# Performance work log

Hardware: AMD Instinct MI355X
Metric: run time of the kernel (lower is better)

The kernel has to match this reference:

```python
import jax, jax.numpy as jnp
import numpy as np

N_NODES = 50000
N_EDGES = 800000
IN_DIM = 128
HIDDEN = 256
N_ETYPES = 13
N_STEPS = 6
NUM_GRAPHS = 64


def setup_inputs() -> dict:
    key = jax.random.key(0)
    ks = jax.random.split(key, 10)
    feat = jax.random.normal(ks[0], (N_NODES, IN_DIM), dtype=jnp.float32)
    W = jax.random.normal(ks[1], (N_ETYPES, HIDDEN, HIDDEN), dtype=jnp.float32) * 0.05
    W_ih = jax.random.normal(ks[2], (3 * HIDDEN, HIDDEN), dtype=jnp.float32) * 0.05
    W_hh = jax.random.normal(ks[3], (3 * HIDDEN, HIDDEN), dtype=jnp.float32) * 0.05
    b_ih = jnp.zeros((3 * HIDDEN,), dtype=jnp.float32)
    b_hh = jnp.zeros((3 * HIDDEN,), dtype=jnp.float32)
    Wc = jax.random.normal(ks[4], (1, HIDDEN), dtype=jnp.float32) * 0.05
    bc = jnp.zeros((1,), dtype=jnp.float32)
    src = jax.random.randint(ks[5], (N_EDGES,), 0, N_NODES, dtype=jnp.int32)
    dst = jax.random.randint(ks[6], (N_EDGES,), 0, N_NODES, dtype=jnp.int32)
    etype = jax.random.randint(ks[7], (N_EDGES,), 0, N_ETYPES, dtype=jnp.int32)
    graph_id = jnp.sort(jax.random.randint(ks[8], (N_NODES,), 0, NUM_GRAPHS, dtype=jnp.int32))
    return {"feat": feat, "W": W, "W_ih": W_ih, "W_hh": W_hh, "b_ih": b_ih,
            "b_hh": b_hh, "Wc": Wc, "bc": bc, "src": src, "dst": dst,
            "etype": etype, "graph_id": graph_id}


def reference(feat, W, W_ih, W_hh, b_ih, b_hh, Wc, bc, src, dst, etype, graph_id):
    N, H = feat.shape[0], W.shape[-1]
    # zero-pad input features to hidden size (DGL GatedGraphConv behaviour)
    h0 = jnp.concatenate([feat, jnp.zeros((N, H - feat.shape[1]), feat.dtype)], axis=1)

    def step(h, _):
        # per-etype linear transform of all nodes: [n_etypes, N, H]
        Th = jnp.einsum('nd,edf->enf', h, W)
        # gather transformed source feature per edge by its edge type: [E, H]
        msg = Th[etype, src]
        # scatter-sum aggregation into destination nodes: [N, H]
        a = jax.ops.segment_sum(msg, dst, num_segments=N)
        # torch.nn.GRUCell(a, h)
        gx = a @ W_ih.T + b_ih
        gh = h @ W_hh.T + b_hh
        xr, xz, xn = jnp.split(gx, 3, axis=-1)
        hr, hz, hn = jnp.split(gh, 3, axis=-1)
        r = jax.nn.sigmoid(xr + hr)
        z = jax.nn.sigmoid(xz + hz)
        n = jnp.tanh(xn + r * hn)
        return (1.0 - z) * n + z * h, None

    h, _ = jax.lax.scan(step, h0, None, length=N_STEPS)
    h = jax.nn.relu(h)
    # dgl.sum_nodes readout per graph: [num_graphs, H]
    hg = jax.ops.segment_sum(h, graph_id, num_segments=NUM_GRAPHS)
    out = jax.nn.sigmoid(hg @ Wc.T + bc)
    return out.squeeze(-1)
```

## Files before the change

kernel.cpp:

```cpp
#include <hip/hip_runtime.h>
#include <math.h>

#define N_NODES   50000
#define N_EDGES   800000
#define IN_DIM    128
#define HIDDEN    256
#define N_ETYPES  13
#define N_STEPS   6
#define NUM_GRAPHS 64
#define NKEYS     (N_ETYPES * N_NODES)
#define SCAN_T    512

typedef __attribute__((ext_vector_type(8))) short bf16x8;
typedef __attribute__((ext_vector_type(4))) float f32x4;
typedef __attribute__((ext_vector_type(4))) unsigned short u16x4;
typedef __attribute__((ext_vector_type(8))) _Float16 f16x8;
typedef __attribute__((ext_vector_type(4))) _Float16 f16x4;

__device__ __forceinline__ float bf2f(unsigned short u) {
    return __uint_as_float((unsigned)u << 16);
}
__device__ __forceinline__ void fsplit(float x, unsigned short& hi, unsigned short& lo) {
    unsigned u = __float_as_uint(x);
    hi = (unsigned short)(u >> 16);
    float l = x - __uint_as_float((u >> 16) << 16);
    lo = (unsigned short)(__float_as_uint(l) >> 16);
}

__global__ __launch_bounds__(256) void k_init_h(const float* __restrict__ feat,
                                                unsigned short* __restrict__ hHi,
                                                unsigned short* __restrict__ hLo,
                                                _Float16* __restrict__ hF16) {
    int i = blockIdx.x * 256 + threadIdx.x;
    if (i >= N_NODES * 64) return;
    int v = i >> 6;
    int q = i & 63;
    float4 val;
    if (q < 32) val = ((const float4*)(feat + (size_t)v * IN_DIM))[q];
    else        val = make_float4(0.f, 0.f, 0.f, 0.f);
    unsigned short h0, l0, h1, l1, h2, l2, h3, l3;
    fsplit(val.x, h0, l0);
    fsplit(val.y, h1, l1);
    fsplit(val.z, h2, l2);
    fsplit(val.w, h3, l3);
    u16x4 hi4, lo4;
    hi4[0] = h0; hi4[1] = h1; hi4[2] = h2; hi4[3] = h3;
    lo4[0] = l0; lo4[1] = l1; lo4[2] = l2; lo4[3] = l3;
    *(u16x4*)(hHi + (size_t)v * 256 + q * 4) = hi4;
    *(u16x4*)(hLo + (size_t)v * 256 + q * 4) = lo4;
    f16x4 f4;
    f4[0] = (_Float16)val.x; f4[1] = (_Float16)val.y;
    f4[2] = (_Float16)val.z; f4[3] = (_Float16)val.w;
    *(f16x4*)(hF16 + (size_t)v * 256 + q * 4) = f4;
}

__global__ __launch_bounds__(256) void k_splitW(const float* __restrict__ W,
                                                short* __restrict__ Whi,
                                                short* __restrict__ Wlo) {
    int i = blockIdx.x * 256 + threadIdx.x;
    if (i >= N_ETYPES * 65536) return;
    int t = i >> 16, rem = i & 65535, n = rem >> 8, k = rem & 255;
    float x = W[(size_t)t * 65536 + k * 256 + n];
    unsigned short hb, lb;
    fsplit(x, hb, lb);
    Whi[i] = (short)hb;
    Wlo[i] = (short)lb;
}

__global__ __launch_bounds__(256) void k_splitLin(const float* __restrict__ Wsrc,
                                                  short* __restrict__ hi,
                                                  short* __restrict__ lo, int n) {
    int i = blockIdx.x * 256 + threadIdx.x;
    if (i >= n) return;
    unsigned short hb, lb;
    fsplit(Wsrc[i], hb, lb);
    hi[i] = (short)hb;
    lo[i] = (short)lb;
}

__global__ __launch_bounds__(256) void k_hist(const int* __restrict__ dst,
                                              const int* __restrict__ et,
                                              int* __restrict__ counts) {
    int e = blockIdx.x * 256 + threadIdx.x;
    if (e >= N_EDGES) return;
    int key = et[e] * N_NODES + dst[e];
    atomicAdd(&counts[key], 1);
}

__global__ __launch_bounds__(SCAN_T) void k_scan1(const int* __restrict__ in,
                                                  int* __restrict__ lexcl,
                                                  int* __restrict__ bsums, int n) {
    __shared__ int s[SCAN_T];
    int i = blockIdx.x * SCAN_T + threadIdx.x;
    int v = (i < n) ? in[i] : 0;
    s[threadIdx.x] = v;
    __syncthreads();
    for (int off = 1; off < SCAN_T; off <<= 1) {
        int t = (threadIdx.x >= off) ? s[threadIdx.x - off] : 0;
        __syncthreads();
        s[threadIdx.x] += t;
        __syncthreads();
    }
    if (i < n) lexcl[i] = s[threadIdx.x] - v;
    if (threadIdx.x == SCAN_T - 1) bsums[blockIdx.x] = s[SCAN_T - 1];
}

__global__ __launch_bounds__(256) void k_scan2(int* __restrict__ bsums, int nb,
                                               int* __restrict__ ptr) {
    __shared__ int s[256];
    int tid = threadIdx.x;
    const int C = (nb + 255) / 256;
    int vals[8];
    int base = tid * C;
    int sum = 0;
    for (int i = 0; i < C; ++i) {
        int idx = base + i;
        int v = (idx < nb) ? bsums[idx] : 0;
        vals[i] = sum;
        sum += v;
    }
    s[tid] = sum;
    __syncthreads();
    int own = sum;
    for (int off = 1; off < 256; off <<= 1) {
        int t = (tid >= off) ? s[tid - off] : 0;
        __syncthreads();
        s[tid] += t;
        __syncthreads();
    }
    int exclBlk = s[tid] - own;
    for (int i = 0; i < C; ++i) {
        int idx = base + i;
        if (idx < nb) bsums[idx] = exclBlk + vals[i];
    }
    if (tid == 0) ptr[NKEYS] = N_EDGES;
}

__global__ __launch_bounds__(SCAN_T) void k_scan3(const int* __restrict__ lexcl,
                                                  const int* __restrict__ bsums,
                                                  int* __restrict__ ptr, int n) {
    int i = blockIdx.x * SCAN_T + threadIdx.x;
    if (i < n) ptr[i] = lexcl[i] + bsums[blockIdx.x];
}

__global__ __launch_bounds__(256) void k_place(const int* __restrict__ dst,
                                               const int* __restrict__ et,
                                               const int* __restrict__ src,
                                               int* __restrict__ cursor,
                                               unsigned* __restrict__ ebuf) {
    int e = blockIdx.x * 256 + threadIdx.x;
    if (e >= N_EDGES) return;
    int d = dst[e];
    int key = et[e] * N_NODES + d;
    int pos = atomicAdd(&cursor[key], 1);
    ebuf[pos] = ((unsigned)d << 16) | (unsigned)src[e];
}

__device__ __forceinline__ void split8(const float4& A, const float4& B,
                                       bf16x8& hi, bf16x8& lo) {
    float x[8] = {A.x, A.y, A.z, A.w, B.x, B.y, B.z, B.w};
    #pragma unroll
    for (int e = 0; e < 8; ++e) {
        unsigned short hb, lb;
        fsplit(x[e], hb, lb);
        hi[e] = (short)hb;
        lo[e] = (short)lb;
    }
}

__global__ __launch_bounds__(256, 4) void k_msg(const unsigned* __restrict__ ebuf,
                                                const int* __restrict__ ptr,
                                                const _Float16* __restrict__ hF16,
                                                const short* __restrict__ Whi,
                                                const short* __restrict__ Wlo,
                                                float* __restrict__ a) {
    __shared__ float4 Sh4[32 * 64];
    const int br   = blockIdx.x * 32;
    const int tid  = threadIdx.x;
    const int l    = tid & 63;
    const int w    = tid >> 6;
    const int ln15 = l & 15;
    const int lhi  = l >> 4;
    const int g    = tid >> 4;
    const int q    = tid & 15;
    float* shf = (float*)Sh4;

    f32x4 acc[2][4] = {};

    for (int t = 0; t < N_ETYPES; ++t) {
        float4 z4 = make_float4(0.f, 0.f, 0.f, 0.f);
        #pragma unroll
        for (int i = 0; i < 8; ++i) Sh4[tid + i * 256] = z4;
        __syncthreads();
        {
            int base = t * N_NODES + br;
            int endk = (br + 32 <= N_NODES) ? (base + 32) : (t * N_NODES + N_NODES);
            int beg  = ptr[base];
            int end  = ptr[endk];
            for (int i = beg + g; i < end; i += 16) {
                unsigned pk = ebuf[i];
                int s = (int)(pk & 0xFFFFu);
                int r = (int)(pk >> 16) - br;
                int sw = r & 7;
                #pragma unroll
                for (int j2 = 0; j2 < 2; ++j2) {
                    const _Float16* vp = hF16 + (size_t)s * 256 + j2 * 128 + q * 8;
                    f16x8 v8 = *reinterpret_cast<const f16x8*>(vp);
                    int c0 = (j2 * 32 + 2 * q) ^ sw;
                    int c1 = (j2 * 32 + 2 * q + 1) ^ sw;
                    float* p0 = shf + ((r * 64 + c0) << 2);
                    float* p1 = shf + ((r * 64 + c1) << 2);
                    atomicAdd(p0 + 0, (float)v8[0]);
                    atomicAdd(p0 + 1, (float)v8[1]);
                    atomicAdd(p0 + 2, (float)v8[2]);
                    atomicAdd(p0 + 3, (float)v8[3]);
                    atomicAdd(p1 + 0, (float)v8[4]);
                    atomicAdd(p1 + 1, (float)v8[5]);
                    atomicAdd(p1 + 2, (float)v8[6]);
                    atomicAdd(p1 + 3, (float)v8[7]);
                }
            }
        }
        __syncthreads();
        const short* WH = Whi + ((size_t)t << 16);
        const short* WL = Wlo + ((size_t)t << 16);
        #pragma unroll 2
        for (int K0 = 0; K0 < 8; ++K0) {
            bf16x8 bh[4], bl[4];
            #pragma unroll
            for (int cb = 0; cb < 4; ++cb) {
                int col = (w << 6) + (cb << 4) + ln15;
                size_t off = (size_t)col * 256 + (K0 << 5) + (lhi << 3);
                bh[cb] = *reinterpret_cast<const bf16x8*>(WH + off);
                bl[cb] = *reinterpret_cast<const bf16x8*>(WL + off);
            }
            #pragma unroll
            for (int rf = 0; rf < 2; ++rf) {
                int row = (rf << 4) + ln15;
                int j0  = (K0 << 3) + (lhi << 1);
                int sw  = row & 7;
                float4 a0 = Sh4[row * 64 + (j0 ^ sw)];
                float4 a1 = Sh4[row * 64 + ((j0 + 1) ^ sw)];
                bf16x8 ah, al;
                split8(a0, a1, ah, al);
                #pragma unroll
                for (int cb = 0; cb < 4; ++cb) {
                    acc[rf][cb] = __builtin_amdgcn_mfma_f32_16x16x32_bf16(ah, bh[cb], acc[rf][cb], 0, 0, 0);
                    acc[rf][cb] = __builtin_amdgcn_mfma_f32_16x16x32_bf16(ah, bl[cb], acc[rf][cb], 0, 0, 0);
                    acc[rf][cb] = __builtin_amdgcn_mfma_f32_16x16x32_bf16(al, bh[cb], acc[rf][cb], 0, 0, 0);
                }
            }
        }
        __syncthreads();
    }
    #pragma unroll
    for (int rf = 0; rf < 2; ++rf) {
        #pragma unroll
        for (int m = 0; m < 4; ++m) {
            int row = br + (rf << 4) + (lhi << 2) + m;
            if (row < N_NODES) {
                #pragma unroll
                for (int cb = 0; cb < 4; ++cb) {
                    int col = (w << 6) + (cb << 4) + ln15;
                    a[(size_t)row * 256 + col] = acc[rf][cb][m];
                }
            }
        }
    }
}

__device__ __forceinline__ float sigm(float x) { return 1.0f / (1.0f + expf(-x)); }

__global__ __launch_bounds__(256, 2) void k_gru(const float* __restrict__ a,
                                                const unsigned short* __restrict__ hHi,
                                                const unsigned short* __restrict__ hLo,
                                                const short* __restrict__ WihH,
                                                const short* __restrict__ WihL,
                                                const short* __restrict__ WhhH,
                                                const short* __restrict__ WhhL,
                                                const float* __restrict__ b_ih,
                                                const float* __restrict__ b_hh,
                                                unsigned short* __restrict__ hNHi,
                                                unsigned short* __restrict__ hNLo,
                                                _Float16* __restrict__ hNF16) {
    const int f0   = blockIdx.x * 64;
    const int br   = blockIdx.y * 64;
    const int tid  = threadIdx.x;
    const int w    = tid >> 6;
    const int l    = tid & 63;
    const int ln15 = l & 15;
    const int lhi  = l >> 4;

    f32x4 accx[3][4] = {};
    f32x4 acch[3][4] = {};

    int rowA = br + (w << 4) + ln15;
    if (rowA >= N_NODES) rowA = N_NODES - 1;
    const float* aRow = a + (size_t)rowA * 256;
    const unsigned short* hHiRow = hHi + (size_t)rowA * 256;
    const unsigned short* hLoRow = hLo + (size_t)rowA * 256;

    #pragma unroll 2
    for (int K0 = 0; K0 < 8; ++K0) {
        const int koff = (K0 << 5) + (lhi << 3);
        float4 av0 = *(const float4*)(aRow + koff);
        float4 av1 = *(const float4*)(aRow + koff + 4);
        bf16x8 aH, aL;
        split8(av0, av1, aH, aL);
        bf16x8 hH = *reinterpret_cast<const bf16x8*>(hHiRow + koff);
        bf16x8 hL = *reinterpret_cast<const bf16x8*>(hLoRow + koff);
        #pragma unroll
        for (int g = 0; g < 3; ++g) {
            #pragma unroll
            for (int cb = 0; cb < 4; ++cb) {
                int col = g * 256 + f0 + (cb << 4) + ln15;
                size_t off = (size_t)col * 256 + koff;
                bf16x8 bH = *reinterpret_cast<const bf16x8*>(WihH + off);
                bf16x8 bL = *reinterpret_cast<const bf16x8*>(WihL + off);
                accx[g][cb] = __builtin_amdgcn_mfma_f32_16x16x32_bf16(aH, bH, accx[g][cb], 0, 0, 0);
                accx[g][cb] = __builtin_amdgcn_mfma_f32_16x16x32_bf16(aH, bL, accx[g][cb], 0, 0, 0);
                accx[g][cb] = __builtin_amdgcn_mfma_f32_16x16x32_bf16(aL, bH, accx[g][cb], 0, 0, 0);
                bH = *reinterpret_cast<const bf16x8*>(WhhH + off);
                bL = *reinterpret_cast<const bf16x8*>(WhhL + off);
                acch[g][cb] = __builtin_amdgcn_mfma_f32_16x16x32_bf16(hH, bH, acch[g][cb], 0, 0, 0);
                acch[g][cb] = __builtin_amdgcn_mfma_f32_16x16x32_bf16(hH, bL, acch[g][cb], 0, 0, 0);
                acch[g][cb] = __builtin_amdgcn_mfma_f32_16x16x32_bf16(hL, bH, acch[g][cb], 0, 0, 0);
            }
        }
    }
    #pragma unroll
    for (int cb = 0; cb < 4; ++cb) {
        int f = f0 + (cb << 4) + ln15;
        float bxr = b_ih[f], bxz = b_ih[256 + f], bxn = b_ih[512 + f];
        float bhr = b_hh[f], bhz = b_hh[256 + f], bhn = b_hh[512 + f];
        #pragma unroll
        for (int m = 0; m < 4; ++m) {
            int row = br + (w << 4) + (lhi << 2) + m;
            if (row >= N_NODES) continue;
            size_t idx = (size_t)row * 256 + f;
            float hv = bf2f(hHi[idx]) + bf2f(hLo[idx]);
            float r = sigm(accx[0][cb][m] + bxr + acch[0][cb][m] + bhr);
            float z = sigm(accx[1][cb][m] + bxz + acch[1][cb][m] + bhz);
            float n = tanhf(accx[2][cb][m] + bxn + r * (acch[2][cb][m] + bhn));
            float o = (1.f - z) * n + z * hv;
            unsigned short ohi, olo;
            fsplit(o, ohi, olo);
            hNHi[idx] = ohi;
            hNLo[idx] = olo;
            hNF16[idx] = (_Float16)o;
        }
    }
}

__global__ __launch_bounds__(256) void k_readout1(const unsigned short* __restrict__ hHi,
                                                  const unsigned short* __restrict__ hLo,
                                                  const int* __restrict__ gid,
                                                  float* __restrict__ hg) {
    int row0 = blockIdx.x * 32;
    if (row0 >= N_NODES) return;
    int f = threadIdx.x;
    int end = row0 + 32; if (end > N_NODES) end = N_NODES;
    float acc = 0.f;
    int cur = gid[row0];
    for (int r = row0; r < end; ++r) {
        int g = gid[r];
        if (g != cur) {
            atomicAdd(&hg[cur * HIDDEN + f], acc);
            acc = 0.f; cur = g;
        }
        size_t idx = (size_t)r * HIDDEN + f;
        float x = bf2f(hHi[idx]) + bf2f(hLo[idx]);
        acc += (x > 0.f) ? x : 0.f;
    }
    atomicAdd(&hg[cur * HIDDEN + f], acc);
}

__global__ __launch_bounds__(256) void k_readout2(const float* __restrict__ hg,
                                                  const float* __restrict__ Wc,
                                                  const float* __restrict__ bc,
                                                  float* __restrict__ out) {
    __shared__ float s[256];
    int g = blockIdx.x;
    int f = threadIdx.x;
    s[f] = hg[g * HIDDEN + f] * Wc[f];
    __syncthreads();
    for (int off = 128; off > 0; off >>= 1) {
        if (f < off) s[f] += s[f + off];
        __syncthreads();
    }
    if (f == 0) out[g] = 1.0f / (1.0f + expf(-(s[0] + bc[0])));
}

extern "C" void kernel_launch(void* const* d_in, const int* in_sizes, int n_in,
                              void* d_out, int out_size, void* d_ws, size_t ws_size,
                              hipStream_t stream) {
    const float* feat  = (const float*)d_in[0];
    const float* W     = (const float*)d_in[1];
    const float* W_ih  = (const float*)d_in[2];
    const float* W_hh  = (const float*)d_in[3];
    const float* b_ih  = (const float*)d_in[4];
    const float* b_hh  = (const float*)d_in[5];
    const float* Wc    = (const float*)d_in[6];
    const float* bc    = (const float*)d_in[7];
    const int*   src   = (const int*)d_in[8];
    const int*   dst   = (const int*)d_in[9];
    const int*   etype = (const int*)d_in[10];
    const int*   gid   = (const int*)d_in[11];
    float* out = (float*)d_out;

    char* ws = (char*)d_ws;
    size_t off = 0;
    auto alloc = [&](size_t bytes) {
        void* p = ws + off;
        off += (bytes + 255) & ~(size_t)255;
        return p;
    };
    unsigned short* hHiA = (unsigned short*)alloc((size_t)N_NODES * HIDDEN * 2);
    unsigned short* hLoA = (unsigned short*)alloc((size_t)N_NODES * HIDDEN * 2);
    unsigned short* hHiB = (unsigned short*)alloc((size_t)N_NODES * HIDDEN * 2);
    unsigned short* hLoB = (unsigned short*)alloc((size_t)N_NODES * HIDDEN * 2);
    _Float16* hF16 = (_Float16*)alloc((size_t)N_NODES * HIDDEN * 2);
    float* a    = (float*)alloc((size_t)N_NODES * HIDDEN * 4);
    int* bufA   = (int*)alloc((size_t)(NKEYS + 1) * 4);
    int* bufB   = (int*)alloc((size_t)NKEYS * 4);
    unsigned* ebuf = (unsigned*)alloc((size_t)N_EDGES * 4);
    int* bsums  = (int*)alloc((size_t)2048 * 4);
    float* hg   = (float*)alloc((size_t)NUM_GRAPHS * HIDDEN * 4);
    short* Whi  = (short*)alloc((size_t)N_ETYPES * 65536 * 2);
    short* Wlo  = (short*)alloc((size_t)N_ETYPES * 65536 * 2);
    short* WihH = (short*)alloc((size_t)768 * 256 * 2);
    short* WihL = (short*)alloc((size_t)768 * 256 * 2);
    short* WhhH = (short*)alloc((size_t)768 * 256 * 2);
    short* WhhL = (short*)alloc((size_t)768 * 256 * 2);
    (void)ws_size; (void)n_in; (void)in_sizes; (void)out_size;

    const int SCAN_BLOCKS = (NKEYS + SCAN_T - 1) / SCAN_T;
    const int NLIN = 768 * 256;

    hipMemsetAsync(bufA, 0, (size_t)NKEYS * 4, stream);
    k_hist<<<(N_EDGES + 255) / 256, 256, 0, stream>>>(dst, etype, bufA);
    k_scan1<<<SCAN_BLOCKS, SCAN_T, 0, stream>>>(bufA, bufB, bsums, NKEYS);
    k_scan2<<<1, 256, 0, stream>>>(bsums, SCAN_BLOCKS, bufA);
    k_scan3<<<SCAN_BLOCKS, SCAN_T, 0, stream>>>(bufB, bsums, bufA, NKEYS);
    hipMemcpyAsync(bufB, bufA, (size_t)NKEYS * 4, hipMemcpyDeviceToDevice, stream);
    k_place<<<(N_EDGES + 255) / 256, 256, 0, stream>>>(dst, etype, src, bufB, ebuf);

    k_splitW<<<(N_ETYPES * 65536 + 255) / 256, 256, 0, stream>>>(W, Whi, Wlo);
    k_splitLin<<<(NLIN + 255) / 256, 256, 0, stream>>>(W_ih, WihH, WihL, NLIN);
    k_splitLin<<<(NLIN + 255) / 256, 256, 0, stream>>>(W_hh, WhhH, WhhL, NLIN);
    k_init_h<<<(N_NODES * 64 + 255) / 256, 256, 0, stream>>>(feat, hHiA, hLoA, hF16);

    unsigned short* hcHi = hHiA; unsigned short* hcLo = hLoA;
    unsigned short* hnHi = hHiB; unsigned short* hnLo = hLoB;
    const dim3 gMsg((N_NODES + 31) / 32, 1);
    const dim3 gGru(HIDDEN / 64, (N_NODES + 63) / 64);

    for (int step = 0; step < N_STEPS; ++step) {
        k_msg<<<gMsg, 256, 0, stream>>>(ebuf, bufA, hF16, Whi, Wlo, a);
        k_gru<<<gGru, 256, 0, stream>>>(a, hcHi, hcLo, WihH, WihL, WhhH, WhhL,
                                        b_ih, b_hh, hnHi, hnLo, hF16);
        unsigned short* t1 = hcHi; hcHi = hnHi; hnHi = t1;
        unsigned short* t2 = hcLo; hcLo = hnLo; hnLo = t2;
    }

    hipMemsetAsync(hg, 0, (size_t)NUM_GRAPHS * HIDDEN * 4, stream);
    k_readout1<<<(N_NODES + 31) / 32, 256, 0, stream>>>(hcHi, hcLo, gid, hg);
    k_readout2<<<NUM_GRAPHS, 256, 0, stream>>>(hg, Wc, bc, out);
}
```

Before: 14.12 ms.

## Split message kernel across edge types with global atomic accumulation

The message kernel now launches one block per (edge type, 32-node tile) pair instead of looping over all 13 edge types inside one block. Each block gathers its edges into shared memory, does the per-type matmul, and atomically adds its partial result into a zeroed global aggregate buffer, which a per-step memset now clears. The gather loop is also remapped so each wavefront handles whole edges with per-lane scalar loads. This raises parallelism and lets blocks stop early when a tile has no edges of that type. In exchange it adds global float atomics on every output element per edge type, an extra memset per step, and order-dependent float summation.

```diff
diff --git a/kernel.cpp b/kernel.cpp
--- a/kernel.cpp
+++ b/kernel.cpp
@@ -168,90 +168,90 @@
     }
 }
 
-__global__ __launch_bounds__(256, 4) void k_msg(const unsigned* __restrict__ ebuf,
-                                                const int* __restrict__ ptr,
-                                                const _Float16* __restrict__ hF16,
-                                                const short* __restrict__ Whi,
-                                                const short* __restrict__ Wlo,
-                                                float* __restrict__ a) {
+__global__ __launch_bounds__(256, 4) void k_msg_et(const unsigned* __restrict__ ebuf,
+                                                   const int* __restrict__ ptr,
+                                                   const _Float16* __restrict__ hF16,
+                                                   const short* __restrict__ Whi,
+                                                   const short* __restrict__ Wlo,
+                                                   float* __restrict__ a) {
     __shared__ float4 Sh4[32 * 64];
-    const int br   = blockIdx.x * 32;
+    const int t    = blockIdx.x;
+    const int br   = blockIdx.y * 32;
     const int tid  = threadIdx.x;
     const int l    = tid & 63;
     const int w    = tid >> 6;
     const int ln15 = l & 15;
     const int lhi  = l >> 4;
-    const int g    = tid >> 4;
-    const int q    = tid & 15;
     float* shf = (float*)Sh4;
 
+    const int base = t * N_NODES + br;
+    const int endk = (br + 32 <= N_NODES) ? (base + 32) : (t * N_NODES + N_NODES);
+    const int beg  = ptr[base];
+    const int end  = ptr[endk];
+    if (beg == end) return;
+
+    float4 z4 = make_float4(0.f, 0.f, 0.f, 0.f);
+    #pragma unroll
+    for (int i = 0; i < 8; ++i) Sh4[tid + i * 256] = z4;
+    __syncthreads();
+
+    for (int i = beg + w; i < end; i += 8) {
+        unsigned pk1 = ebuf[i];
+        int i2 = i + 4;
+        int has2 = i2 < end;
+        unsigned pk2 = has2 ? ebuf[i2] : pk1;
+        int s1 = (int)(pk1 & 0xFFFFu), r1 = (int)(pk1 >> 16) - br;
+        int s2 = (int)(pk2 & 0xFFFFu), r2 = (int)(pk2 >> 16) - br;
+        float v1[4], v2[4];
+        #pragma unroll
+        for (int j = 0; j < 4; ++j) v1[j] = (float)hF16[(size_t)s1 * 256 + 64 * j + l];
+        #pragma unroll
+        for (int j = 0; j < 4; ++j) v2[j] = (float)hF16[(size_t)s2 * 256 + 64 * j + l];
+        int sw1 = r1 & 7, sw2 = r2 & 7;
+        #pragma unroll
+        for (int j = 0; j < 4; ++j) {
+            int c = 64 * j + l;
+            atomicAdd(shf + r1 * 256 + (((c >> 2) ^ sw1) << 2) + (c & 3), v1[j]);
+        }
+        if (has2) {
+            #pragma unroll
+            for (int j = 0; j < 4; ++j) {
+                int c = 64 * j + l;
+                atomicAdd(shf + r2 * 256 + (((c >> 2) ^ sw2) << 2) + (c & 3), v2[j]);
+            }
+        }
+    }
+    __syncthreads();
+
     f32x4 acc[2][4] = {};
-
-    for (int t = 0; t < N_ETYPES; ++t) {
-        float4 z4 = make_float4(0.f, 0.f, 0.f, 0.f);
-        #pragma unroll
-        for (int i = 0; i < 8; ++i) Sh4[tid + i * 256] = z4;
-        __syncthreads();
-        {
-            int base = t * N_NODES + br;
-            int endk = (br + 32 <= N_NODES) ? (base + 32) : (t * N_NODES + N_NODES);
-            int beg  = ptr[base];
-            int end  = ptr[endk];
-            for (int i = beg + g; i < end; i += 16) {
-                unsigned pk = ebuf[i];
-                int s = (int)(pk & 0xFFFFu);
-                int r = (int)(pk >> 16) - br;
-                int sw = r & 7;
-                #pragma unroll
-                for (int j2 = 0; j2 < 2; ++j2) {
-                    const _Float16* vp = hF16 + (size_t)s * 256 + j2 * 128 + q * 8;
-                    f16x8 v8 = *reinterpret_cast<const f16x8*>(vp);
-                    int c0 = (j2 * 32 + 2 * q) ^ sw;
-                    int c1 = (j2 * 32 + 2 * q + 1) ^ sw;
-                    float* p0 = shf + ((r * 64 + c0) << 2);
-                    float* p1 = shf + ((r * 64 + c1) << 2);
-                    atomicAdd(p0 + 0, (float)v8[0]);
-                    atomicAdd(p0 + 1, (float)v8[1]);
-                    atomicAdd(p0 + 2, (float)v8[2]);
-                    atomicAdd(p0 + 3, (float)v8[3]);
-                    atomicAdd(p1 + 0, (float)v8[4]);
-                    atomicAdd(p1 + 1, (float)v8[5]);
-                    atomicAdd(p1 + 2, (float)v8[6]);
-                    atomicAdd(p1 + 3, (float)v8[7]);
-                }
-            }
-        }
-        __syncthreads();
-        const short* WH = Whi + ((size_t)t << 16);
-        const short* WL = Wlo + ((size_t)t << 16);
-        #pragma unroll 2
-        for (int K0 = 0; K0 < 8; ++K0) {
-            bf16x8 bh[4], bl[4];
+    const short* WH = Whi + ((size_t)t << 16);
+    const short* WL = Wlo + ((size_t)t << 16);
+    #pragma unroll 2
+    for (int K0 = 0; K0 < 8; ++K0) {
+        bf16x8 bh[4], bl[4];
+        #pragma unroll
+        for (int cb = 0; cb < 4; ++cb) {
+            int col = (w << 6) + (cb << 4) + ln15;
+            size_t off = (size_t)col * 256 + (K0 << 5) + (lhi << 3);
+            bh[cb] = *reinterpret_cast<const bf16x8*>(WH + off);
+            bl[cb] = *reinterpret_cast<const bf16x8*>(WL + off);
+        }
+        #pragma unroll
+        for (int rf = 0; rf < 2; ++rf) {
+            int row = (rf << 4) + ln15;
+            int j0  = (K0 << 3) + (lhi << 1);
+            int sw  = row & 7;
+            float4 a0 = Sh4[row * 64 + (j0 ^ sw)];
+            float4 a1 = Sh4[row * 64 + ((j0 + 1) ^ sw)];
+            bf16x8 ah, al;
+            split8(a0, a1, ah, al);
             #pragma unroll
             for (int cb = 0; cb < 4; ++cb) {
-                int col = (w << 6) + (cb << 4) + ln15;
-                size_t off = (size_t)col * 256 + (K0 << 5) + (lhi << 3);
-                bh[cb] = *reinterpret_cast<const bf16x8*>(WH + off);
-                bl[cb] = *reinterpret_cast<const bf16x8*>(WL + off);
+                acc[rf][cb] = __builtin_amdgcn_mfma_f32_16x16x32_bf16(ah, bh[cb], acc[rf][cb], 0, 0, 0);
+                acc[rf][cb] = __builtin_amdgcn_mfma_f32_16x16x32_bf16(ah, bl[cb], acc[rf][cb], 0, 0, 0);
+                acc[rf][cb] = __builtin_amdgcn_mfma_f32_16x16x32_bf16(al, bh[cb], acc[rf][cb], 0, 0, 0);
             }
-            #pragma unroll
-            for (int rf = 0; rf < 2; ++rf) {
-                int row = (rf << 4) + ln15;
-                int j0  = (K0 << 3) + (lhi << 1);
-                int sw  = row & 7;
-                float4 a0 = Sh4[row * 64 + (j0 ^ sw)];
-                float4 a1 = Sh4[row * 64 + ((j0 + 1) ^ sw)];
-                bf16x8 ah, al;
-                split8(a0, a1, ah, al);
-                #pragma unroll
-                for (int cb = 0; cb < 4; ++cb) {
-                    acc[rf][cb] = __builtin_amdgcn_mfma_f32_16x16x32_bf16(ah, bh[cb], acc[rf][cb], 0, 0, 0);
-                    acc[rf][cb] = __builtin_amdgcn_mfma_f32_16x16x32_bf16(ah, bl[cb], acc[rf][cb], 0, 0, 0);
-                    acc[rf][cb] = __builtin_amdgcn_mfma_f32_16x16x32_bf16(al, bh[cb], acc[rf][cb], 0, 0, 0);
-                }
-            }
-        }
-        __syncthreads();
+        }
     }
     #pragma unroll
     for (int rf = 0; rf < 2; ++rf) {
@@ -262,7 +262,7 @@
                 #pragma unroll
                 for (int cb = 0; cb < 4; ++cb) {
                     int col = (w << 6) + (cb << 4) + ln15;
-                    a[(size_t)row * 256 + col] = acc[rf][cb][m];
+                    atomicAdd(a + (size_t)row * 256 + col, acc[rf][cb][m]);
                 }
             }
         }
@@ -452,11 +452,12 @@
 
     unsigned short* hcHi = hHiA; unsigned short* hcLo = hLoA;
     unsigned short* hnHi = hHiB; unsigned short* hnLo = hLoB;
-    const dim3 gMsg((N_NODES + 31) / 32, 1);
+    const dim3 gMsg(N_ETYPES, (N_NODES + 31) / 32);
     const dim3 gGru(HIDDEN / 64, (N_NODES + 63) / 64);
 
     for (int step = 0; step < N_STEPS; ++step) {
-        k_msg<<<gMsg, 256, 0, stream>>>(ebuf, bufA, hF16, Whi, Wlo, a);
+        hipMemsetAsync(a, 0, (size_t)N_NODES * HIDDEN * 4, stream);
+        k_msg_et<<<gMsg, 256, 0, stream>>>(ebuf, bufA, hF16, Whi, Wlo, a);
         k_gru<<<gGru, 256, 0, stream>>>(a, hcHi, hcLo, WihH, WihL, WhhH, WhhL,
                                         b_ih, b_hh, hnHi, hnLo, hF16);
         unsigned short* t1 = hcHi; hcHi = hnHi; hnHi = t1;
```

After: 11.67 ms. 1.21x faster.
